# Kernel tuning notes

Hardware: AMD Instinct MI355X
Metric: run time of the kernel (lower is better)

## Reference

```python
import jax, jax.numpy as jnp
import numpy as np

F_FILT = 40      # num_filters
K_GABOR = 401    # n_coefficients
K_POOL = 401     # window_length
HOP = 160        # hop_length
SR = 16000
EPS_PCEN = 1e-6
EPS_IN = 1e-5    # nn.InstanceNorm1d default eps
B, T = 8, 160000


def _hz2mel(f):
    return 2595.0 * np.log10(1.0 + f / 700.0)


def _mel2hz(m):
    return 700.0 * (10.0 ** (m / 2595.0) - 1.0)


def setup_inputs() -> dict:
    key = jax.random.key(0)
    x = jax.random.normal(key, (B, 1, T), dtype=jnp.float32)
    # mel-spaced Gabor center frequencies / bandwidths (filter_init_method='mel')
    edges = _mel2hz(np.linspace(_hz2mel(60.0), _hz2mel(7800.0), F_FILT + 2))
    center = edges[1:-1]
    fwhm = np.maximum(edges[2:] - edges[:-2], 1.0)
    eta = 2.0 * np.pi * center / SR                      # rad/sample
    sigma = np.sqrt(2.0 * np.log(2.0)) / (np.pi * fwhm / SR)  # samples
    ones = jnp.ones(F_FILT, jnp.float32)
    return {
        "x": x,
        "gabor_eta": jnp.asarray(eta, jnp.float32),
        "gabor_sigma": jnp.asarray(sigma, jnp.float32),
        "pool_bandwidths": 0.4 * ones,   # GaussianLowPass init
        "pool_bias": ones,               # GaussianLowPass bias init (ones)
        "ema_weights": 0.04 * ones,      # sPCEN smoothing_coefficient, per-channel
        "alpha": 0.96 * ones,
        "delta": 2.0 * ones,
        "root": 0.96 * ones,             # root=compression_factor=0.96
    }


def _conv1d(x, w, stride=1, groups=1):
    # x: (N, C, T), w: (O, C//groups, K); cross-correlation like torch F.conv1d
    return jax.lax.conv_general_dilated(
        x, w, (stride,), "VALID",
        dimension_numbers=("NCH", "OIH", "NCH"),
        feature_group_count=groups)


def _ema_scan(x, s):
    # y_0 = x_0 ; y_t = s*x_t + (1-s)*y_{t-1}  (per-channel s), parallel scan
    s3 = s[None, :, None]
    a = jnp.broadcast_to(1.0 - s3, x.shape)
    b = s3 * x
    a = a.at[:, :, 0].set(0.0)
    b = b.at[:, :, 0].set(x[:, :, 0])
    def comb(c1, c2):
        a1, b1 = c1
        a2, b2 = c2
        return a1 * a2, a2 * b1 + b2
    _, y = jax.lax.associative_scan(comb, (a, b), axis=2)
    return y


def reference(x, gabor_eta, gabor_sigma, pool_bandwidths, pool_bias,
              ema_weights, alpha, delta, root):
    dt = x.dtype
    # --- Gabor complex conv frontend -> |.|^2 ---
    t = jnp.arange(K_GABOR, dtype=dt) - (K_GABOR - 1) / 2.0
    env = jnp.exp(-0.5 * (t[None] / gabor_sigma[:, None]) ** 2) \
          / (jnp.sqrt(2.0 * jnp.pi) * gabor_sigma[:, None])
    phase = gabor_eta[:, None] * t[None]
    kern = jnp.stack([env * jnp.cos(phase), env * jnp.sin(phase)], axis=1)
    kern = kern.reshape(2 * F_FILT, 1, K_GABOR)
    xp = jnp.pad(x, ((0, 0), (0, 0), (K_GABOR - 1, 0)))  # causal pad
    y = _conv1d(xp, kern)                                 # (B, 2F, T)
    y = y.reshape(y.shape[0], F_FILT, 2, y.shape[-1])
    power = y[:, :, 0] ** 2 + y[:, :, 1] ** 2             # |z|^2, (B, F, T)

    # --- sPCEN compression ---
    s = jnp.clip(ema_weights, 0.0, 1.0)
    ema = _ema_scan(power, s)
    a3 = jnp.minimum(alpha, 1.0)[None, :, None]
    inv_r = (1.0 / jnp.maximum(root, 1.0))[None, :, None]
    d3 = delta[None, :, None]
    comp = (power / (EPS_PCEN + ema) ** a3 + d3) ** inv_r - d3 ** inv_r

    # --- Gaussian low-pass depthwise pooling (causal, stride=HOP) ---
    bw = jnp.clip(pool_bandwidths, 2.0 / K_POOL, 0.5)
    tp = jnp.arange(-K_POOL // 2, K_POOL // 2, dtype=dt)  # -201..199, len 401
    den = bw * 0.5 * (K_POOL - 1)
    pk = jnp.exp(-0.5 * (tp[None] / den[:, None]) ** 2).reshape(F_FILT, 1, K_POOL)
    cp = jnp.pad(comp, ((0, 0), (0, 0), (K_POOL - 1, 0)))
    pooled = _conv1d(cp, pk, stride=HOP, groups=F_FILT) + pool_bias[None, :, None]

    # --- InstanceNorm1d (affine=False, biased var, eps=1e-5) ---
    m = pooled.mean(-1, keepdims=True)
    v = pooled.var(-1, keepdims=True)
    return (pooled - m) / jnp.sqrt(v + EPS_IN)
```

## Files before the change

kernel.cpp:

```cpp
#include <hip/hip_runtime.h>
#include <math.h>

#define F_FILT   40
#define K_GABOR  401
#define HOP      160
#define T_LEN    160000
#define B_BATCH  8
#define EPS_PCENF 1e-6f
#define EPS_INF   1e-5f

#define NG       5
#define GF       8
#define NKMAX    13
#define TC       640
#define UW       10
#define NCH1     250
#define NSTG     136
#define PHS      548

#define PC_THREADS 256
#define PC_NWAVES  4
#define SPAN     6400
#define WTILE    640
#define W_NT     10
#define NSP      25
#define RT       10
#define KP       208
#define HALOP    200
#define RINGW    520
#define WSTR     728

typedef _Float16 h2_t  __attribute__((ext_vector_type(2)));
typedef _Float16 half8 __attribute__((ext_vector_type(8)));
typedef float    f32x4 __attribute__((ext_vector_type(4)));

__device__ __forceinline__ float fdot2(h2_t a, h2_t b, float c) {
    return __builtin_amdgcn_fdot2(a, b, c, false);
}
__device__ __forceinline__ unsigned pk2(float a, float b) {
    return __builtin_bit_cast(unsigned, __builtin_amdgcn_cvt_pkrtz(a, b));
}
__device__ __forceinline__ h2_t bch(unsigned u) {
    return __builtin_bit_cast(h2_t, u);
}
__device__ __forceinline__ float fexp2(float x) { return __builtin_amdgcn_exp2f(x); }
__device__ __forceinline__ float flog2(float x) { return __builtin_amdgcn_logf(x); }

__device__ __forceinline__ void group_span(float sigma0, int& klo, int& nk) {
    const int R = min(200, (int)ceilf(4.5f * sigma0));
    klo = (200 - R) & ~31;
    nk  = ((200 + R - klo) >> 5) + 1;
    if (nk > NKMAX) nk = NKMAX;
}

__global__ __launch_bounds__(256) void leaf_weights(
    const float* __restrict__ eta_g, const float* __restrict__ sigma_g,
    const float* __restrict__ bw_g,
    _Float16* __restrict__ Atab, unsigned* __restrict__ pktab)
{
    const int gi = blockIdx.x;
    const int f0 = gi * GF;
    int klo, nk;
    group_span(sigma_g[f0], klo, nk);

    for (int idx = threadIdx.x; idx < 52 * 16 * 8; idx += 256) {
        const int c8 = idx >> 7;
        const int m  = (idx >> 3) & 15;
        const int i  = idx & 7;
        const int f  = f0 + (m >> 1);
        const int k  = klo + c8 * 8 + i;
        float w = 0.f;
        if (k <= 400) {
            const float sg = sigma_g[f];
            const float t  = (float)(k - 200);
            const float z  = t / sg;
            const float e  = (0.3989422804014327f / sg) * expf(-0.5f * z * z);
            const float ph = eta_g[f] * t;
            w = (m & 1) ? e * sinf(ph) : e * cosf(ph);
        }
        Atab[(size_t)(gi * 52 + c8) * 128 + m * 8 + i] = (_Float16)w;
    }
    for (int idx = threadIdx.x; idx < GF * KP; idx += 256) {
        const int fl = idx / KP, i = idx % KP;
        const int f = f0 + fl;
        const float bw  = fminf(fmaxf(bw_g[f], 2.0f / 401.0f), 0.5f);
        const float den = bw * 0.5f * 400.0f;
        float pp[2];
        for (int j = 0; j < 2; ++j) {
            int k = 2 * i + j;
            float pv = 0.f;
            if (k < K_GABOR) {
                float tp = (float)(k - 201);
                float d = tp / den;
                pv = expf(-0.5f * d * d);
            }
            pp[j] = pv;
        }
        pktab[f * KP + i] = pk2(pp[0], pp[1]);
    }
}

template<int NK>
__device__ __forceinline__ void conv_kloop(
    const uint4* __restrict__ ph4, const uint4* __restrict__ Ap,
    int aBase, int pbase, f32x4* acc)
{
    uint4 F[UW];
#pragma unroll
    for (int u = 0; u < UW; ++u) F[u] = ph4[pbase + 2 * u];
#pragma unroll
    for (int jk = 0; jk < NK; ++jk) {
        const half8 aCur = __builtin_bit_cast(half8, Ap[aBase + jk * 64]);
#pragma unroll
        for (int u = 0; u < UW; ++u) {
            acc[u] = __builtin_amdgcn_mfma_f32_16x16x32_f16(
                aCur, __builtin_bit_cast(half8, F[(2 * jk + u) % UW]), acc[u], 0, 0, 0);
        }
        if (jk + 1 < NK) {
            F[(2 * jk) % UW]     = ph4[pbase + 4 * (jk + 1) + 16];
            F[(2 * jk + 1) % UW] = ph4[pbase + 4 * (jk + 1) + 18];
        }
    }
}

__global__ __launch_bounds__(256) void leaf_conv(
    const float* __restrict__ x,
    const float* __restrict__ sigma_g,
    const _Float16* __restrict__ Atab,
    _Float16* __restrict__ Pall)
{
    __shared__ unsigned ph[8 * PHS];

    const int gi = blockIdx.x % NG;
    const int ch = (blockIdx.x / NG) % NCH1;
    const int b  = blockIdx.x / (NG * NCH1);
    const int f0 = gi * GF;
    const int tid = threadIdx.x;
    const int lane = tid & 63;
    const int w    = tid >> 6;

    const float* __restrict__ xb = x + (size_t)b * T_LEN;
    _Float16* __restrict__ Pb = Pall + (size_t)b * F_FILT * T_LEN;

    int klo, nk;
    group_span(sigma_g[f0], klo, nk);
    const int t0   = ch * TC;
    const int base = t0 + klo - 400;

    if (tid < NSTG) {
        const int g0 = base + 8 * tid;
        float v[15];
        if (g0 >= 0 && g0 + 14 < T_LEN) {
            const float4 a0 = *(const float4*)(xb + g0);
            const float4 a1 = *(const float4*)(xb + g0 + 4);
            const float4 a2 = *(const float4*)(xb + g0 + 8);
            const float4 a3 = *(const float4*)(xb + g0 + 12);
            v[0]=a0.x; v[1]=a0.y; v[2]=a0.z; v[3]=a0.w;
            v[4]=a1.x; v[5]=a1.y; v[6]=a1.z; v[7]=a1.w;
            v[8]=a2.x; v[9]=a2.y; v[10]=a2.z; v[11]=a2.w;
            v[12]=a3.x; v[13]=a3.y; v[14]=a3.z;
        } else {
#pragma unroll
            for (int e = 0; e < 15; ++e) {
                const int gidx = g0 + e;
                v[e] = (gidx >= 0 && gidx < T_LEN) ? xb[gidx] : 0.f;
            }
        }
        unsigned pw[14];
#pragma unroll
        for (int s = 0; s < 14; ++s) pw[s] = pk2(v[s], v[s + 1]);
#pragma unroll
        for (int r = 0; r < 8; ++r) {
            uint4 fr;
            fr.x = pw[r]; fr.y = pw[r + 2]; fr.z = pw[r + 4]; fr.w = pw[r + 6];
            *(uint4*)&ph[r * PHS + 4 * tid] = fr;
        }
    }
    __syncthreads();

    const int n  = lane & 15;
    const int kb = lane >> 4;
    const int q  = n + 8 * kb + 160 * w;
    const int pbase = (q & 7) * (PHS / 4) + (q >> 3);

    f32x4 acc[UW];
#pragma unroll
    for (int u = 0; u < UW; ++u) acc[u] = (f32x4){0.f, 0.f, 0.f, 0.f};

    const uint4* ph4 = (const uint4*)ph;
    const uint4* Ap = (const uint4*)Atab;
    const int aBase = (gi * 52 + kb) * 16 + n;

    switch (nk) {
        case 3:  conv_kloop<3>(ph4, Ap, aBase, pbase, acc); break;
        case 4:  conv_kloop<4>(ph4, Ap, aBase, pbase, acc); break;
        case 5:  conv_kloop<5>(ph4, Ap, aBase, pbase, acc); break;
        case 6:
        case 7:  conv_kloop<7>(ph4, Ap, aBase, pbase, acc); break;
        case 8:
        case 9:  conv_kloop<9>(ph4, Ap, aBase, pbase, acc); break;
        default: conv_kloop<13>(ph4, Ap, aBase, pbase, acc); break;
    }

    const int g  = lane >> 4;
    const int fA = f0 + 2 * g;
#pragma unroll
    for (int u = 0; u < UW; ++u) {
        const int t = t0 + (w * UW + u) * 16 + n;
        const float P0 = acc[u].x * acc[u].x + acc[u].y * acc[u].y;
        const float P1 = acc[u].z * acc[u].z + acc[u].w * acc[u].w;
        Pb[(size_t)fA * T_LEN + t]       = (_Float16)P0;
        Pb[(size_t)(fA + 1) * T_LEN + t] = (_Float16)P1;
    }
}

__global__ __launch_bounds__(PC_THREADS) void leaf_pcen(
    const _Float16* __restrict__ Pall,
    const float* __restrict__ bias_g,
    const float* __restrict__ ema_g,
    const float* __restrict__ alpha_g,
    const float* __restrict__ delta_g,
    const float* __restrict__ root_g,
    const unsigned* __restrict__ pktab,
    float* __restrict__ outp)
{
    __shared__ unsigned lds[PC_NWAVES * WSTR];

    const int tid  = threadIdx.x;
    const int lane = tid & 63;
    const int wv   = tid >> 6;
    const int wid  = blockIdx.x * PC_NWAVES + wv;
    const int sp   = wid % NSP;
    const int bf   = wid / NSP;
    const int f    = bf % F_FILT;

    unsigned* ring = lds + wv * WSTR;
    unsigned* pkl  = ring + RINGW;

    const float sw    = fminf(fmaxf(ema_g[f], 0.0f), 1.0f);
    const float a     = 1.0f - sw;
    const float alpha = fminf(alpha_g[f], 1.0f);
    const float inv_r = 1.0f / fmaxf(root_g[f], 1.0f);
    const float dlt   = delta_g[f];
    const float dpow  = fexp2(inv_r * flog2(dlt));
    const bool  rt1   = (inv_r == 1.0f);
    const float bias  = bias_g[f];

    for (int i = lane; i < KP; i += 64) pkl[i] = pktab[f * KP + i];
    for (int i = lane; i < HALOP; i += 64) ring[i] = 0u;

    const float a2 = a * a, a4 = a2 * a2, a8 = a4 * a4;
    const float A1  = a8 * a2;
    const float A2  = A1 * A1, A4 = A2 * A2, A8 = A4 * A4;
    const float A16 = A8 * A8, A32 = A16 * A16, A64 = A32 * A32;
    float Al = 1.0f;
    if (lane & 1)  Al *= A1;
    if (lane & 2)  Al *= A2;
    if (lane & 4)  Al *= A4;
    if (lane & 8)  Al *= A8;
    if (lane & 16) Al *= A16;
    if (lane & 32) Al *= A32;

    const unsigned* PU = (const unsigned*)(Pall + (size_t)bf * T_LEN);
    const int wbase = sp * (SPAN / 2);
    const int itStart = (sp == 0) ? 0 : -1;
    float carry = 0.f;

    unsigned sv[5];
    {
        const int tb = wbase + itStart * 320 + lane * 5;
#pragma unroll
        for (int q = 0; q < 5; ++q) sv[q] = PU[tb + q];
    }

    for (int it = itStart; it < W_NT; ++it) {
        float p[RT];
#pragma unroll
        for (int q = 0; q < 5; ++q) {
            const h2_t hh = bch(sv[q]);
            p[2 * q]     = (float)hh.x;
            p[2 * q + 1] = (float)hh.y;
        }
        {
            const int nt = it + 1;
            const int tb = wbase + (nt < W_NT ? nt : 0) * 320 + lane * 5;
#pragma unroll
            for (int q = 0; q < 5; ++q) sv[q] = PU[tb + q];
        }

        float up[RT];
        float uu = 0.f;
#pragma unroll
        for (int r = 0; r < RT; ++r) {
            uu = fmaf(a, uu, sw * p[r]);
            up[r] = uu;
        }

        float cc = carry;
        if (sp == 0 && it == 0) cc = __shfl(p[0], 0);

        float v = uu;
        {
            float tv;
            tv = __shfl_up(v, 1);  if (lane >= 1)  v = fmaf(A1,  tv, v);
            tv = __shfl_up(v, 2);  if (lane >= 2)  v = fmaf(A2,  tv, v);
            tv = __shfl_up(v, 4);  if (lane >= 4)  v = fmaf(A4,  tv, v);
            tv = __shfl_up(v, 8);  if (lane >= 8)  v = fmaf(A8,  tv, v);
            tv = __shfl_up(v, 16); if (lane >= 16) v = fmaf(A16, tv, v);
            tv = __shfl_up(v, 32); if (lane >= 32) v = fmaf(A32, tv, v);
        }
        const float vlast = __shfl(v, 63);
        float cin;
        {
            float ve = __shfl_up(v, 1);
            if (lane == 0) ve = 0.f;
            cin = fmaf(Al, cc, ve);
        }
        carry = fmaf(A64, cc, vlast);

        float apr = a;
#pragma unroll
        for (int j = 0; j < 5; ++j) {
            const float e0 = fmaf(apr, cin, up[2 * j]);     apr *= a;
            const float e1 = fmaf(apr, cin, up[2 * j + 1]); apr *= a;
            const float d0 = fexp2(-alpha * flog2(EPS_PCENF + e0));
            const float d1 = fexp2(-alpha * flog2(EPS_PCENF + e1));
            float c0, c1;
            if (rt1) {
                c0 = p[2 * j] * d0;
                c1 = p[2 * j + 1] * d1;
            } else {
                const float q0 = fmaf(p[2 * j],     d0, dlt);
                const float q1 = fmaf(p[2 * j + 1], d1, dlt);
                c0 = fexp2(inv_r * flog2(q0)) - dpow;
                c1 = fexp2(inv_r * flog2(q1)) - dpow;
            }
            ring[HALOP + lane * 5 + j] = pk2(c0, c1);
        }

        if (it >= 0) {
            const int o = lane >> 4, l = lane & 15;
            float part = 0.f;
#pragma unroll
            for (int t = 0; t < 13; ++t) {
                const int kpp = l + 16 * t;
                part = fdot2(bch(ring[o * 80 + kpp]), bch(pkl[kpp]), part);
            }
            part += __shfl_xor(part, 1, 16);
            part += __shfl_xor(part, 2, 16);
            part += __shfl_xor(part, 4, 16);
            part += __shfl_xor(part, 8, 16);
            if (l == 0)
                outp[(size_t)bf * 1000 + sp * (W_NT * 4) + it * 4 + o] = part + bias;
        }

        for (int i = lane; i < HALOP; i += 64) ring[i] = ring[320 + i];
    }
}

__global__ __launch_bounds__(256) void leaf_norm(float* __restrict__ out)
{
    const int bf = blockIdx.x;
    float* p = out + (size_t)bf * 1000;
    __shared__ float buf[1000];
    __shared__ float red[4];
    const int tid = threadIdx.x;
    const int lane = tid & 63, wave = tid >> 6;

    float sum = 0.0f;
    for (int i = tid; i < 1000; i += 256) { float v = p[i]; buf[i] = v; sum += v; }
    for (int m = 1; m < 64; m <<= 1) sum += __shfl_xor(sum, m);
    if (lane == 0) red[wave] = sum;
    __syncthreads();
    const float mean = (red[0] + red[1] + red[2] + red[3]) * 0.001f;

    float vs = 0.0f;
    for (int i = tid; i < 1000; i += 256) { float d = buf[i] - mean; vs += d * d; }
    for (int m = 1; m < 64; m <<= 1) vs += __shfl_xor(vs, m);
    __syncthreads();
    if (lane == 0) red[wave] = vs;
    __syncthreads();
    const float var   = (red[0] + red[1] + red[2] + red[3]) * 0.001f;
    const float scale = rsqrtf(var + EPS_INF);
    for (int i = tid; i < 1000; i += 256) p[i] = (buf[i] - mean) * scale;
}

extern "C" void kernel_launch(void* const* d_in, const int* in_sizes, int n_in,
                              void* d_out, int out_size, void* d_ws, size_t ws_size,
                              hipStream_t stream)
{
    const float* x     = (const float*)d_in[0];
    const float* eta   = (const float*)d_in[1];
    const float* sigma = (const float*)d_in[2];
    const float* bw    = (const float*)d_in[3];
    const float* bias  = (const float*)d_in[4];
    const float* emaw  = (const float*)d_in[5];
    const float* alpha = (const float*)d_in[6];
    const float* delta = (const float*)d_in[7];
    const float* root  = (const float*)d_in[8];
    float* outp = (float*)d_out;

    _Float16* Atab  = (_Float16*)d_ws;
    unsigned* pktab = (unsigned*)((char*)d_ws + 133120);
    _Float16* Pall  = (_Float16*)((char*)d_ws + 166400);

    hipLaunchKernelGGL(leaf_weights, dim3(NG), dim3(256), 0, stream,
                       eta, sigma, bw, Atab, pktab);
    hipLaunchKernelGGL(leaf_conv, dim3(B_BATCH * NG * NCH1), dim3(256), 0, stream,
                       x, sigma, Atab, Pall);
    hipLaunchKernelGGL(leaf_pcen, dim3(B_BATCH * F_FILT * NSP / PC_NWAVES), dim3(PC_THREADS),
                       0, stream, Pall, bias, emaw, alpha, delta, root, pktab, outp);
    hipLaunchKernelGGL(leaf_norm, dim3(B_BATCH * F_FILT), dim3(256), 0, stream, outp);
}
```

Before: 105.0 us.

## Interleave filter-pair power into packed half2 rows and narrow Gabor tap span

The conv kernel now writes each pair of adjacent filters' power as one packed half2 word per time step, replacing two scattered half stores. The PCEN kernel reads these packed rows and selects its component, so each wave loads twice the bytes it uses. Separately, the Gabor truncation radius shrinks from 4.5 to 4.0 sigma, which cuts MFMA k-chunks for some groups. The narrower support drops small tail contributions and can change accuracy.

```diff
diff --git a/kernel.cpp b/kernel.cpp
--- a/kernel.cpp
+++ b/kernel.cpp
@@ -21,7 +21,6 @@
 #define PC_THREADS 256
 #define PC_NWAVES  4
 #define SPAN     6400
-#define WTILE    640
 #define W_NT     10
 #define NSP      25
 #define RT       10
@@ -47,7 +46,7 @@
 __device__ __forceinline__ float flog2(float x) { return __builtin_amdgcn_logf(x); }
 
 __device__ __forceinline__ void group_span(float sigma0, int& klo, int& nk) {
-    const int R = min(200, (int)ceilf(4.5f * sigma0));
+    const int R = min(200, (int)ceilf(4.0f * sigma0));
     klo = (200 - R) & ~31;
     nk  = ((200 + R - klo) >> 5) + 1;
     if (nk > NKMAX) nk = NKMAX;
@@ -127,7 +126,7 @@
     const float* __restrict__ x,
     const float* __restrict__ sigma_g,
     const _Float16* __restrict__ Atab,
-    _Float16* __restrict__ Pall)
+    unsigned* __restrict__ P2all)
 {
     __shared__ unsigned ph[8 * PHS];
 
@@ -140,7 +139,7 @@
     const int w    = tid >> 6;
 
     const float* __restrict__ xb = x + (size_t)b * T_LEN;
-    _Float16* __restrict__ Pb = Pall + (size_t)b * F_FILT * T_LEN;
+    unsigned* __restrict__ Pb2 = P2all + (size_t)b * 20 * T_LEN;
 
     int klo, nk;
     group_span(sigma_g[f0], klo, nk);
@@ -203,19 +202,18 @@
     }
 
     const int g  = lane >> 4;
-    const int fA = f0 + 2 * g;
+    unsigned* __restrict__ Prow = Pb2 + (size_t)(gi * 4 + g) * T_LEN;
 #pragma unroll
     for (int u = 0; u < UW; ++u) {
         const int t = t0 + (w * UW + u) * 16 + n;
         const float P0 = acc[u].x * acc[u].x + acc[u].y * acc[u].y;
         const float P1 = acc[u].z * acc[u].z + acc[u].w * acc[u].w;
-        Pb[(size_t)fA * T_LEN + t]       = (_Float16)P0;
-        Pb[(size_t)(fA + 1) * T_LEN + t] = (_Float16)P1;
+        Prow[t] = pk2(P0, P1);
     }
 }
 
 __global__ __launch_bounds__(PC_THREADS) void leaf_pcen(
-    const _Float16* __restrict__ Pall,
+    const unsigned* __restrict__ P2all,
     const float* __restrict__ bias_g,
     const float* __restrict__ ema_g,
     const float* __restrict__ alpha_g,
@@ -233,6 +231,8 @@
     const int sp   = wid % NSP;
     const int bf   = wid / NSP;
     const int f    = bf % F_FILT;
+    const int b    = bf / F_FILT;
+    const int comp = f & 1;
 
     unsigned* ring = lds + wv * WSTR;
     unsigned* pkl  = ring + RINGW;
@@ -261,31 +261,30 @@
     if (lane & 16) Al *= A16;
     if (lane & 32) Al *= A32;
 
-    const unsigned* PU = (const unsigned*)(Pall + (size_t)bf * T_LEN);
-    const int wbase = sp * (SPAN / 2);
+    const unsigned* PU = P2all + ((size_t)b * 20 + (f >> 1)) * T_LEN;
+    const int sbase = sp * SPAN;
     const int itStart = (sp == 0) ? 0 : -1;
     float carry = 0.f;
 
-    unsigned sv[5];
+    unsigned sv[RT];
     {
-        const int tb = wbase + itStart * 320 + lane * 5;
-#pragma unroll
-        for (int q = 0; q < 5; ++q) sv[q] = PU[tb + q];
+        const int tb = sbase + itStart * 640 + lane * 10;
+#pragma unroll
+        for (int q = 0; q < RT; ++q) sv[q] = PU[tb + q];
     }
 
     for (int it = itStart; it < W_NT; ++it) {
         float p[RT];
 #pragma unroll
-        for (int q = 0; q < 5; ++q) {
+        for (int q = 0; q < RT; ++q) {
             const h2_t hh = bch(sv[q]);
-            p[2 * q]     = (float)hh.x;
-            p[2 * q + 1] = (float)hh.y;
+            p[q] = comp ? (float)hh.y : (float)hh.x;
         }
         {
             const int nt = it + 1;
-            const int tb = wbase + (nt < W_NT ? nt : 0) * 320 + lane * 5;
-#pragma unroll
-            for (int q = 0; q < 5; ++q) sv[q] = PU[tb + q];
+            const int tb = sbase + (nt < W_NT ? nt : 0) * 640 + lane * 10;
+#pragma unroll
+            for (int q = 0; q < RT; ++q) sv[q] = PU[tb + q];
         }
 
         float up[RT];
@@ -402,13 +401,13 @@
 
     _Float16* Atab  = (_Float16*)d_ws;
     unsigned* pktab = (unsigned*)((char*)d_ws + 133120);
-    _Float16* Pall  = (_Float16*)((char*)d_ws + 166400);
+    unsigned* P2all = (unsigned*)((char*)d_ws + 166400);
 
     hipLaunchKernelGGL(leaf_weights, dim3(NG), dim3(256), 0, stream,
                        eta, sigma, bw, Atab, pktab);
     hipLaunchKernelGGL(leaf_conv, dim3(B_BATCH * NG * NCH1), dim3(256), 0, stream,
-                       x, sigma, Atab, Pall);
+                       x, sigma, Atab, P2all);
     hipLaunchKernelGGL(leaf_pcen, dim3(B_BATCH * F_FILT * NSP / PC_NWAVES), dim3(PC_THREADS),
-                       0, stream, Pall, bias, emaw, alpha, delta, root, pktab, outp);
+                       0, stream, P2all, bias, emaw, alpha, delta, root, pktab, outp);
     hipLaunchKernelGGL(leaf_norm, dim3(B_BATCH * F_FILT), dim3(256), 0, stream, outp);
 }
```

Result: slower. 111.1 us (+5.8%).
